# Optimization experiments

Measured on AMD Instinct MI355X. Metric: run time of the kernel, lower is better.

## Reference

```python
import jax, jax.numpy as jnp
import numpy as np

ALPHA = 0.2      # LeakyReLU negative slope for GAT attention
EPS = 1e-6       # LayerNorm eps (custom LayerNorm: (x-mean)/(std+eps)*g+b, unbiased std)
B, L, E, H, D = 16, 1024, 128, 4, 128
N = L + 1        # nodes = codes + appended target node


def leaky(x):
    return jnp.where(x >= 0, x, ALPHA * x)


def layer_norm(x, g, b):
    mu = jnp.mean(x, axis=-1, keepdims=True)
    sd = jnp.std(x, axis=-1, ddof=1, keepdims=True)
    return g * (x - mu) / (sd + EPS) + b


def masked_softmax(logits, mask):
    # logits broadcastable to mask shape [..., N, N]; mask in {0,1}
    l = jnp.where(mask > 0, logits, jnp.asarray(-1e9, logits.dtype))
    a = jax.nn.softmax(l, axis=-1)
    # nodes with no incoming edges aggregate nothing (sparse-GAT semantics)
    has_edge = (jnp.sum(mask, axis=-1, keepdims=True) > 0).astype(a.dtype)
    return a * has_edge


def setup_inputs() -> dict:
    key = jax.random.key(0)
    ks = jax.random.split(key, 20)
    s = 0.1
    HE = H * E
    inp = {}
    inp['data'] = jax.random.randint(ks[0], (B, L), 0, 2).astype(jnp.int32)
    inp['embed'] = jax.random.normal(ks[1], (N, E), jnp.float32) * s
    inp['W_enc'] = jax.random.normal(ks[2], (H, E, E), jnp.float32) * s
    inp['a_enc_src'] = jax.random.normal(ks[3], (H, E), jnp.float32) * s
    inp['a_enc_dst'] = jax.random.normal(ks[4], (H, E), jnp.float32) * s
    inp['g_enc'] = jnp.ones((HE,), jnp.float32)
    inp['b_enc'] = jnp.zeros((HE,), jnp.float32)
    inp['W_dec'] = jax.random.normal(ks[5], (H, HE, D), jnp.float32) * s
    inp['a_dec_src'] = jax.random.normal(ks[6], (H, D), jnp.float32) * s
    inp['a_dec_dst'] = jax.random.normal(ks[7], (H, D), jnp.float32) * s
    inp['g_dec'] = jnp.ones((D,), jnp.float32)
    inp['b_dec'] = jnp.zeros((D,), jnp.float32)
    inp['V_w'] = jax.random.normal(ks[8], (D, D), jnp.float32) * s
    inp['V_b'] = jnp.zeros((D,), jnp.float32)
    inp['o1_w'] = jax.random.normal(ks[9], (D, D), jnp.float32) * s
    inp['o1_b'] = jnp.zeros((D,), jnp.float32)
    inp['o2_w'] = jax.random.normal(ks[10], (D, 1), jnp.float32) * s
    inp['o2_b'] = jnp.zeros((1,), jnp.float32)
    return inp


def reference(data, embed, W_enc, a_enc_src, a_enc_dst, g_enc, b_enc,
              W_dec, a_dec_src, a_dec_dst, g_dec, b_dec,
              V_w, V_b, o1_w, o1_b, o2_w, o2_b):
    emb = embed.at[0].set(0.0)                       # padding_idx=0
    z = (data != 0).astype(emb.dtype)                # [B,L] nonzero indicator
    z_in = jnp.pad(z, ((0, 0), (0, 1)))              # target node absent from input graph
    z_out = jnp.pad(z, ((0, 0), (0, 1)), constant_values=1.0)  # target node added
    mask_in = z_in[:, :, None] * z_in[:, None, :]    # [B,N,N] complete graph over nonzero set
    mask_out = z_out[:, :, None] * z_out[:, None, :]

    # ---- encoder GAT heads (node features shared across batch) ----
    Wh = jnp.einsum('ne,hef->hnf', emb, W_enc)       # [H,N,E]
    f1 = jnp.einsum('hnf,hf->hn', Wh, a_enc_src)
    f2 = jnp.einsum('hnf,hf->hn', Wh, a_enc_dst)
    logits = leaky(f1[:, :, None] + f2[:, None, :])  # [H,N,N], batch-independent
    att = masked_softmax(logits[None], mask_in[:, None])   # [B,H,N,N]
    enc = jax.nn.elu(jnp.einsum('bhij,hjf->bhif', att, Wh))  # concat=True -> ELU
    enc = enc.transpose(0, 2, 1, 3).reshape(data.shape[0], N, -1)  # [B,N,H*E]
    enc = jax.nn.elu(layer_norm(enc, g_enc, b_enc))

    # ---- decoder GAT heads (concat=False -> mean over heads, no ELU) ----
    Wh2 = jnp.einsum('bne,hef->bhnf', enc, W_dec)    # [B,H,N,D]
    g1 = jnp.einsum('bhnf,hf->bhn', Wh2, a_dec_src)
    g2 = jnp.einsum('bhnf,hf->bhn', Wh2, a_dec_dst)
    logits2 = leaky(g1[..., :, None] + g2[..., None, :])   # [B,H,N,N]
    att2 = masked_softmax(logits2, mask_out[:, None])
    dec = jnp.einsum('bhij,bhjf->bhif', att2, Wh2).mean(axis=1)  # [B,N,D]

    dec = jax.nn.relu(layer_norm(dec, g_dec, b_dec)) @ V_w + V_b
    x = dec[:, -1, :]                                # target node per sample
    h = jax.nn.relu(x @ o1_w + o1_b)
    pred = h @ o2_w + o2_b                           # [B,1]
    return pred
```

## Files before the change

kernel.cpp:

```cpp
#include <hip/hip_runtime.h>
#include <hip/hip_bf16.h>

#define BB 16
#define LL 1024
#define EE 128
#define HH 4
#define DD 128
#define NN 1025
#define HE 512
#define AL 0.2f
#define EPSV 1e-6f
#define SS 8
#define CC 128
#define C1 129

#define O_WH   0
#define O_F1   524800
#define O_F2   528900
#define O_ELO  537096
#define O_EHI  541192
#define O_EF1H 545288
#define O_EF1L 549384
#define O_W2   553480
#define O_SLO  555528
#define O_SHI  1612296
#define O_SLOS 2669064
#define O_SHIS 2677320
#define O_WR   2685576
#define O_UP   2751112
#define O_JS   3799688
#define O_PS   3803784
#define O_E4   3807880
#define O_TLO  3807880
#define O_THI  4864648
#define O_TLOS 5921416
#define O_THIS 5929672
#define O_U    4856456
#define O_ZA   4889224
#define O_DP   4889352

__global__ void VGNN_27049704030896_kernel(const float* __restrict__ embed,
                                           const float* __restrict__ W_enc,
                                           const float* __restrict__ a_src,
                                           const float* __restrict__ a_dst,
                                           float* __restrict__ Wh,
                                           float* __restrict__ f1,
                                           float* __restrict__ f2,
                                           float* __restrict__ ef1hi,
                                           float* __restrict__ ef1lo) {
  __shared__ float red[8][EE];
  int n0 = blockIdx.x * 4;
  int h = blockIdx.y;
  int f = threadIdx.x;
  const float* ep0 = embed + (long)((n0 + 0 < NN) ? n0 + 0 : NN - 1) * EE;
  const float* ep1 = embed + (long)((n0 + 1 < NN) ? n0 + 1 : NN - 1) * EE;
  const float* ep2 = embed + (long)((n0 + 2 < NN) ? n0 + 2 : NN - 1) * EE;
  const float* ep3 = embed + (long)((n0 + 3 < NN) ? n0 + 3 : NN - 1) * EE;
  float m0 = (n0 + 0 > 0 && n0 + 0 < NN) ? 1.0f : 0.0f;
  float m1 = (n0 + 1 > 0 && n0 + 1 < NN) ? 1.0f : 0.0f;
  float m2 = (n0 + 2 > 0 && n0 + 2 < NN) ? 1.0f : 0.0f;
  float m3 = (n0 + 3 > 0 && n0 + 3 < NN) ? 1.0f : 0.0f;
  float a0 = 0.0f, a1 = 0.0f, a2 = 0.0f, a3 = 0.0f;
  for (int e = 0; e < EE; e++) {
    float wv = W_enc[((long)(h * EE + e)) * EE + f];
    a0 += ep0[e] * wv; a1 += ep1[e] * wv;
    a2 += ep2[e] * wv; a3 += ep3[e] * wv;
  }
  a0 *= m0; a1 *= m1; a2 *= m2; a3 *= m3;
  if (n0 + 0 < NN) Wh[((long)(h * NN + n0 + 0)) * EE + f] = a0;
  if (n0 + 1 < NN) Wh[((long)(h * NN + n0 + 1)) * EE + f] = a1;
  if (n0 + 2 < NN) Wh[((long)(h * NN + n0 + 2)) * EE + f] = a2;
  if (n0 + 3 < NN) Wh[((long)(h * NN + n0 + 3)) * EE + f] = a3;
  float asv = a_src[h * EE + f];
  float adv = a_dst[h * EE + f];
  red[0][f] = a0 * asv; red[1][f] = a0 * adv;
  red[2][f] = a1 * asv; red[3][f] = a1 * adv;
  red[4][f] = a2 * asv; red[5][f] = a2 * adv;
  red[6][f] = a3 * asv; red[7][f] = a3 * adv;
  __syncthreads();
  for (int s = 64; s > 0; s >>= 1) {
    if (f < s) {
#pragma unroll
      for (int k = 0; k < 8; k++) red[k][f] += red[k][f + s];
    }
    __syncthreads();
  }
  if (f < 4) {
    int n = n0 + f;
    if (n < NN) {
      float v1 = red[2 * f][0];
      float v2 = red[2 * f + 1][0];
      f1[h * NN + n] = v1;
      f2[h * NN + n] = v2;
      if (n < LL) {
        ef1hi[h * LL + n] = expf(v1);
        ef1lo[h * LL + n] = expf(AL * v1);
      }
    }
  }
}

__global__ void k_rank(const float* __restrict__ f2, const float* __restrict__ f1,
                       int* __restrict__ jsort, float* __restrict__ elo,
                       float* __restrict__ ehi, int* __restrict__ pstar) {
  __shared__ float key[LL];
  int h = blockIdx.x;
  int blk = blockIdx.y;
  int t = threadIdx.x;
  for (int q = t; q < LL; q += 128) key[q] = f2[h * NN + q];
  __syncthreads();
  int j0 = blk * 128 + t;
  float kv = key[j0];
  float tg = -f1[h * NN + j0];
  int rank = 0, cnt = 0;
  for (int q = 0; q < LL; q += 4) {
    float4 k4 = *(const float4*)&key[q];
    rank += ((k4.x < kv) || (k4.x == kv && (q + 0) < j0)) ? 1 : 0;
    rank += ((k4.y < kv) || (k4.y == kv && (q + 1) < j0)) ? 1 : 0;
    rank += ((k4.z < kv) || (k4.z == kv && (q + 2) < j0)) ? 1 : 0;
    rank += ((k4.w < kv) || (k4.w == kv && (q + 3) < j0)) ? 1 : 0;
    cnt += (k4.x < tg) ? 1 : 0;
    cnt += (k4.y < tg) ? 1 : 0;
    cnt += (k4.z < tg) ? 1 : 0;
    cnt += (k4.w < tg) ? 1 : 0;
  }
  jsort[h * LL + rank] = j0;
  elo[h * LL + rank] = expf(AL * kv);
  ehi[h * LL + rank] = expf(kv);
  pstar[h * LL + j0] = cnt;
}

__global__ void k_scanA(const int* __restrict__ data, const int* __restrict__ jsort,
                        const float* __restrict__ elo, const float* __restrict__ ehi,
                        const float* __restrict__ Wh,
                        float* __restrict__ TotLo, float* __restrict__ TotHi,
                        float* __restrict__ TotLoS, float* __restrict__ TotHiS) {
  int c = blockIdx.x;
  int h = blockIdx.y;
  int b = blockIdx.z;
  int t = threadIdx.x;
  int bh = b * HH + h;
  float al0 = 0.0f, al1 = 0.0f, ah0 = 0.0f, ah1 = 0.0f, sl = 0.0f, sh = 0.0f;
  for (int r = 0; r < SS; r++) {
    int p = c * SS + r;
    int j = jsort[h * LL + p];
    if (data[b * LL + j] != 0) {
      float wl = elo[h * LL + p];
      float wh = ehi[h * LL + p];
      float2 v = *(const float2*)&Wh[((long)(h * NN + j)) * EE + 2 * t];
      al0 += wl * v.x; al1 += wl * v.y;
      ah0 += wh * v.x; ah1 += wh * v.y;
      sl += wl; sh += wh;
    }
  }
  long o = (long)(bh * C1 + c);
  float2 s;
  s.x = al0; s.y = al1; *(float2*)&TotLo[o * EE + 2 * t] = s;
  s.x = ah0; s.y = ah1; *(float2*)&TotHi[o * EE + 2 * t] = s;
  if (t == 0) { TotLoS[o] = sl; TotHiS[o] = sh; }
}

__global__ void k_scanB(const float* __restrict__ TotLo, const float* __restrict__ TotHi,
                        const float* __restrict__ TotLoS, const float* __restrict__ TotHiS,
                        float* __restrict__ SnapLo, float* __restrict__ SnapHi,
                        float* __restrict__ SnapLoS, float* __restrict__ SnapHiS) {
  int bh = blockIdx.x;
  int f = threadIdx.x & 127;
  int a = threadIdx.x >> 7;
  const float* __restrict__ T  = a ? TotHi  : TotLo;
  const float* __restrict__ Ts = a ? TotHiS : TotLoS;
  float* __restrict__ S  = a ? SnapHi  : SnapLo;
  float* __restrict__ Ss = a ? SnapHiS : SnapLoS;
  float r = 0.0f, rs = 0.0f;
#pragma unroll 8
  for (int c = 0; c < CC; c++) {
    long o = (long)(bh * C1 + c);
    float tv = T[o * EE + f];
    float ts = Ts[o];
    S[o * EE + f] = r;
    if (f == 0) Ss[o] = rs;
    r += tv; rs += ts;
  }
  long o = (long)(bh * C1 + CC);
  S[o * EE + f] = r;
  if (f == 0) Ss[o] = rs;
}

__global__ void k_w2(const float* __restrict__ W_dec, const float* __restrict__ a_vec,
                     float* __restrict__ w2) {
  int k = blockIdx.x * 128 + threadIdx.x;
  int h = blockIdx.y;
  const float4* wp = (const float4*)&W_dec[(long)(h * HE + k) * DD];
  const float4* ap = (const float4*)&a_vec[h * DD];
  float s = 0.0f;
  for (int d = 0; d < DD / 4; d++) {
    float4 wv = wp[d];
    float4 av = ap[d];
    s += wv.x * av.x + wv.y * av.y + wv.z * av.z + wv.w * av.w;
  }
  w2[h * HE + k] = s;
}

__global__ void k_row(const int* __restrict__ data, const float* __restrict__ Wh,
                      const int* __restrict__ pstar, const int* __restrict__ jsort,
                      const float* __restrict__ elo, const float* __restrict__ ehi,
                      const float* __restrict__ ef1hi, const float* __restrict__ ef1lo,
                      const float* __restrict__ SnapLo, const float* __restrict__ SnapHi,
                      const float* __restrict__ SnapLoS, const float* __restrict__ SnapHiS,
                      const float* __restrict__ g_enc, const float* __restrict__ b_enc,
                      const float* __restrict__ w2,
                      __hip_bfloat16* __restrict__ enc4, float* __restrict__ wrow) {
  int i = blockIdx.x;
  int b = blockIdx.y;
  int t = threadIdx.x;
  if (data[b * LL + i] == 0) {
    if (t < HH) wrow[(b * HH + t) * LL + i] = 0.0f;
    return;
  }
  float x0[HH];
  float x1[HH];
  for (int h = 0; h < HH; h++) {
    int p = pstar[h * LL + i];
    int c = p / SS;
    int bh = b * HH + h;
    long o = (long)(bh * C1 + c);
    float2 rl = *(const float2*)&SnapLo[o * EE + 2 * t];
    float2 rh = *(const float2*)&SnapHi[o * EE + 2 * t];
    float rls = SnapLoS[o];
    float rhs = SnapHiS[o];
    int q0 = c * SS;
    int np = p - q0;
#pragma unroll
    for (int r = 0; r < 7; r++) {
      if (r < np) {
        int j = jsort[h * LL + q0 + r];
        if (data[b * LL + j] != 0) {
          float wl = elo[h * LL + q0 + r];
          float wh2 = ehi[h * LL + q0 + r];
          float2 v = *(const float2*)&Wh[((long)(h * NN + j)) * EE + 2 * t];
          rl.x += wl * v.x; rl.y += wl * v.y;
          rh.x += wh2 * v.x; rh.y += wh2 * v.y;
          rls += wl; rhs += wh2;
        }
      }
    }
    long ot = (long)(bh * C1 + CC);
    float2 Th = *(const float2*)&SnapHi[ot * EE + 2 * t];
    float Ths = SnapHiS[ot];
    float eh = ef1hi[h * LL + i];
    float el = ef1lo[h * LL + i];
    float den = 1.0f / (eh * (Ths - rhs) + el * rls);
    float v0 = (eh * (Th.x - rh.x) + el * rl.x) * den;
    float v1 = (eh * (Th.y - rh.y) + el * rl.y) * den;
    x0[h] = (v0 > 0.0f) ? v0 : (expf(v0) - 1.0f);
    x1[h] = (v1 > 0.0f) ? v1 : (expf(v1) - 1.0f);
  }
  float loc = 0.0f;
  for (int h = 0; h < HH; h++) loc += x0[h] + x1[h];
#pragma unroll
  for (int s = 1; s < 64; s <<= 1) loc += __shfl_xor(loc, s, 64);
  float mu = loc * (1.0f / 512.0f);
  float q2 = 0.0f;
  for (int h = 0; h < HH; h++) {
    float d0 = x0[h] - mu;
    float d1 = x1[h] - mu;
    q2 += d0 * d0 + d1 * d1;
  }
#pragma unroll
  for (int s = 1; s < 64; s <<= 1) q2 += __shfl_xor(q2, s, 64);
  float inv = 1.0f / (sqrtf(q2 * (1.0f / 511.0f)) + EPSV);
  float e40[HH];
  float e41[HH];
  long rowo = ((long)(b * LL + i)) * HE;
  for (int h = 0; h < HH; h++) {
    float2 g = *(const float2*)&g_enc[h * EE + 2 * t];
    float2 bb = *(const float2*)&b_enc[h * EE + 2 * t];
    float v0 = g.x * (x0[h] - mu) * inv + bb.x;
    float v1 = g.y * (x1[h] - mu) * inv + bb.y;
    e40[h] = (v0 > 0.0f) ? v0 : (expf(v0) - 1.0f);
    e41[h] = (v1 > 0.0f) ? v1 : (expf(v1) - 1.0f);
    __hip_bfloat162 pk;
    pk.x = __float2bfloat16(e40[h]);
    pk.y = __float2bfloat16(e41[h]);
    *(__hip_bfloat162*)&enc4[rowo + h * EE + 2 * t] = pk;
  }
  float p0 = 0.0f, p1 = 0.0f, p2 = 0.0f, p3 = 0.0f;
  for (int h = 0; h < HH; h++) {
    float2 wA = *(const float2*)&w2[0 * HE + h * EE + 2 * t];
    float2 wB = *(const float2*)&w2[1 * HE + h * EE + 2 * t];
    float2 wC = *(const float2*)&w2[2 * HE + h * EE + 2 * t];
    float2 wD = *(const float2*)&w2[3 * HE + h * EE + 2 * t];
    p0 += e40[h] * wA.x + e41[h] * wA.y;
    p1 += e40[h] * wB.x + e41[h] * wB.y;
    p2 += e40[h] * wC.x + e41[h] * wC.y;
    p3 += e40[h] * wD.x + e41[h] * wD.y;
  }
#pragma unroll
  for (int s = 1; s < 64; s <<= 1) {
    p0 += __shfl_xor(p0, s, 64);
    p1 += __shfl_xor(p1, s, 64);
    p2 += __shfl_xor(p2, s, 64);
    p3 += __shfl_xor(p3, s, 64);
  }
  if (t < HH) {
    float g = (t == 0) ? p0 : (t == 1) ? p1 : (t == 2) ? p2 : p3;
    if (g < 0.0f) g *= AL;
    wrow[(b * HH + t) * LL + i] = expf(g);
  }
}

__global__ void k_acc(const int* __restrict__ data, const __hip_bfloat16* __restrict__ enc4,
                      const float* __restrict__ wrow, float* __restrict__ Upart) {
  int c = blockIdx.x;
  int b = blockIdx.y;
  int t = threadIdx.x;
  float a00 = 0.0f, a01 = 0.0f, a10 = 0.0f, a11 = 0.0f;
  float a20 = 0.0f, a21 = 0.0f, a30 = 0.0f, a31 = 0.0f;
  for (int r = 0; r < 64; r++) {
    int i = c * 64 + r;
    if (data[b * LL + i] == 0) continue;
    float w0 = wrow[(b * HH + 0) * LL + i];
    float w1 = wrow[(b * HH + 1) * LL + i];
    float w2v = wrow[(b * HH + 2) * LL + i];
    float w3 = wrow[(b * HH + 3) * LL + i];
    __hip_bfloat162 pk = *(const __hip_bfloat162*)&enc4[((long)(b * LL + i)) * HE + 2 * t];
    float e0 = __bfloat162float(pk.x);
    float e1 = __bfloat162float(pk.y);
    a00 += w0 * e0; a01 += w0 * e1;
    a10 += w1 * e0; a11 += w1 * e1;
    a20 += w2v * e0; a21 += w2v * e1;
    a30 += w3 * e0; a31 += w3 * e1;
  }
  long base = (long)(b * 16 + c) * (HH * HE);
  float2 s;
  s.x = a00; s.y = a01; *(float2*)&Upart[base + 0 * HE + 2 * t] = s;
  s.x = a10; s.y = a11; *(float2*)&Upart[base + 1 * HE + 2 * t] = s;
  s.x = a20; s.y = a21; *(float2*)&Upart[base + 2 * HE + 2 * t] = s;
  s.x = a30; s.y = a31; *(float2*)&Upart[base + 3 * HE + 2 * t] = s;
}

__global__ void k_usum(const float* __restrict__ Upart, const float* __restrict__ wrow,
                       float* __restrict__ U, float* __restrict__ zacc) {
  __shared__ float red[256];
  int b = blockIdx.x;
  int t = threadIdx.x;
  for (int k = t; k < HH * HE; k += 256) {
    float s = 0.0f;
    for (int c = 0; c < 16; c++) {
      s += Upart[(long)(b * 16 + c) * (HH * HE) + k];
    }
    U[b * (HH * HE) + k] = s;
  }
  for (int hp = 0; hp < HH; hp++) {
    float p = 0.0f;
    for (int q = t; q < LL; q += 256) p += wrow[(b * HH + hp) * LL + q];
    red[t] = p;
    __syncthreads();
    for (int s = 128; s > 0; s >>= 1) {
      if (t < s) red[t] += red[t + s];
      __syncthreads();
    }
    if (t == 0) zacc[b * HH + hp] = red[0];
    __syncthreads();
  }
}

__global__ void k_dmv(const float* __restrict__ U, const float* __restrict__ zacc,
                      const float* __restrict__ W_dec, float* __restrict__ decPart) {
  __shared__ float Uc[128];
  int cK = blockIdx.x;
  int b = blockIdx.y;
  int f = threadIdx.x;
  int k0 = cK * 128;
  int h = cK / 4;
  Uc[f] = U[b * (HH * HE) + k0 + f];
  __syncthreads();
  float zinv = 1.0f / (1.0f + zacc[b * HH + h]);
  float s = 0.0f;
  for (int kk = 0; kk < 128; kk++) {
    s += Uc[kk] * W_dec[(long)(k0 + kk) * DD + f];
  }
  decPart[(long)(b * 16 + cK) * DD + f] = 0.25f * s * zinv;
}

__global__ void k_finB(const float* __restrict__ decPart,
                       const float* __restrict__ g_dec, const float* __restrict__ b_dec,
                       const float* __restrict__ V_w, const float* __restrict__ V_b,
                       const float* __restrict__ o1_w, const float* __restrict__ o1_b,
                       const float* __restrict__ o2_w, const float* __restrict__ o2_b,
                       float* __restrict__ out) {
  __shared__ float red[DD];
  __shared__ float xs[DD];
  int b = blockIdx.x;
  int f = threadIdx.x;
  float dec = 0.0f;
  for (int cK = 0; cK < 16; cK++) {
    dec += decPart[(long)(b * 16 + cK) * DD + f];
  }
  red[f] = dec;
  __syncthreads();
  for (int s = 64; s > 0; s >>= 1) {
    if (f < s) red[f] += red[f + s];
    __syncthreads();
  }
  float mu = red[0] / 128.0f;
  __syncthreads();
  float dd = dec - mu;
  red[f] = dd * dd;
  __syncthreads();
  for (int s = 64; s > 0; s >>= 1) {
    if (f < s) red[f] += red[f + s];
    __syncthreads();
  }
  float sd = sqrtf(red[0] / 127.0f);
  float t = g_dec[f] * dd / (sd + EPSV) + b_dec[f];
  if (t < 0.0f) t = 0.0f;
  __syncthreads();
  xs[f] = t;
  __syncthreads();
  float xv = 0.0f;
  for (int k = 0; k < DD; k++) xv += xs[k] * V_w[k * DD + f];
  xv += V_b[f];
  __syncthreads();
  xs[f] = xv;
  __syncthreads();
  float hv = 0.0f;
  for (int k = 0; k < DD; k++) hv += xs[k] * o1_w[k * DD + f];
  hv += o1_b[f];
  if (hv < 0.0f) hv = 0.0f;
  red[f] = hv * o2_w[f];
  __syncthreads();
  for (int s = 64; s > 0; s >>= 1) {
    if (f < s) red[f] += red[f + s];
    __syncthreads();
  }
  if (f == 0) out[b] = red[0] + o2_b[0];
}

extern "C" void kernel_launch(void* const* d_in, const int* in_sizes, int n_in,
                              void* d_out, int out_size, void* d_ws, size_t ws_size,
                              hipStream_t stream) {
  const int* data    = (const int*)d_in[0];
  const float* embed  = (const float*)d_in[1];
  const float* W_enc  = (const float*)d_in[2];
  const float* a_esrc = (const float*)d_in[3];
  const float* a_edst = (const float*)d_in[4];
  const float* g_enc  = (const float*)d_in[5];
  const float* b_enc  = (const float*)d_in[6];
  const float* W_dec  = (const float*)d_in[7];
  const float* a_ddst = (const float*)d_in[9];
  const float* g_dec  = (const float*)d_in[10];
  const float* b_dec  = (const float*)d_in[11];
  const float* V_w    = (const float*)d_in[12];
  const float* V_b    = (const float*)d_in[13];
  const float* o1_w   = (const float*)d_in[14];
  const float* o1_b   = (const float*)d_in[15];
  const float* o2_w   = (const float*)d_in[16];
  const float* o2_b   = (const float*)d_in[17];
  float* out = (float*)d_out;

  float* w = (float*)d_ws;
  float* Wh    = w + O_WH;
  float* f1    = w + O_F1;
  float* f2    = w + O_F2;
  float* elo   = w + O_ELO;
  float* ehi   = w + O_EHI;
  float* ef1hi = w + O_EF1H;
  float* ef1lo = w + O_EF1L;
  float* w2    = w + O_W2;
  float* SnapLo  = w + O_SLO;
  float* SnapHi  = w + O_SHI;
  float* SnapLoS = w + O_SLOS;
  float* SnapHiS = w + O_SHIS;
  float* TotLo   = w + O_TLO;
  float* TotHi   = w + O_THI;
  float* TotLoS  = w + O_TLOS;
  float* TotHiS  = w + O_THIS;
  float* wrow  = w + O_WR;
  float* Upart = w + O_UP;
  int* jsort   = (int*)(w + O_JS);
  int* pstar   = (int*)(w + O_PS);
  __hip_bfloat16* enc4 = (__hip_bfloat16*)(w + O_E4);
  float* U     = w + O_U;
  float* zacc  = w + O_ZA;
  float* decPart = w + O_DP;

  VGNN_27049704030896_kernel<<<dim3((NN + 3) / 4, HH), 128, 0, stream>>>(
      embed, W_enc, a_esrc, a_edst, Wh, f1, f2, ef1hi, ef1lo);
  k_rank<<<dim3(HH, LL / 128), 128, 0, stream>>>(f2, f1, jsort, elo, ehi, pstar);
  k_scanA<<<dim3(CC, HH, BB), 64, 0, stream>>>(data, jsort, elo, ehi, Wh,
                                               TotLo, TotHi, TotLoS, TotHiS);
  k_scanB<<<BB * HH, 256, 0, stream>>>(TotLo, TotHi, TotLoS, TotHiS,
                                       SnapLo, SnapHi, SnapLoS, SnapHiS);
  k_w2  <<<dim3(HE / 128, HH), 128, 0, stream>>>(W_dec, a_ddst, w2);
  k_row <<<dim3(LL, BB), 64, 0, stream>>>(data, Wh, pstar, jsort, elo, ehi,
                                          ef1hi, ef1lo, SnapLo, SnapHi,
                                          SnapLoS, SnapHiS, g_enc, b_enc, w2,
                                          enc4, wrow);
  k_acc <<<dim3(16, BB), 256, 0, stream>>>(data, enc4, wrow, Upart);
  k_usum<<<BB, 256, 0, stream>>>(Upart, wrow, U, zacc);
  k_dmv <<<dim3(16, BB), 128, 0, stream>>>(U, zacc, W_dec, decPart);
  k_finB<<<BB, 128, 0, stream>>>(decPart, g_dec, b_dec, V_w, V_b,
                                 o1_w, o1_b, o2_w, o2_b, out);
}
```

Measured before the change: 237.6 us.

## Fuse decoder tail kernels into one per-batch block and merge w2 into rank

Merges the k_w2 projection into the rank kernel as extra blocks. Replaces four tail kernels (accumulate, partial sum, decoder matvec, final MLP) with a single 1024-thread block per batch that reduces in shared memory. This removes several launches and global round-trips for partial buffers. In exchange, the enc4 accumulation now runs on only 16 blocks instead of 256, which reduces parallelism over a large memory read.

```diff
diff --git a/kernel.cpp b/kernel.cpp
--- a/kernel.cpp
+++ b/kernel.cpp
@@ -27,7 +27,6 @@
 #define O_SLOS 2669064
 #define O_SHIS 2677320
 #define O_WR   2685576
-#define O_UP   2751112
 #define O_JS   3799688
 #define O_PS   3803784
 #define O_E4   3807880
@@ -35,9 +34,6 @@
 #define O_THI  4864648
 #define O_TLOS 5921416
 #define O_THIS 5929672
-#define O_U    4856456
-#define O_ZA   4889224
-#define O_DP   4889352
 
 __global__ void VGNN_27049704030896_kernel(const float* __restrict__ embed,
                                            const float* __restrict__ W_enc,
@@ -100,13 +96,31 @@
   }
 }
 
-__global__ void k_rank(const float* __restrict__ f2, const float* __restrict__ f1,
-                       int* __restrict__ jsort, float* __restrict__ elo,
-                       float* __restrict__ ehi, int* __restrict__ pstar) {
+__global__ void k_rankw2(const float* __restrict__ f2, const float* __restrict__ f1,
+                         const float* __restrict__ W_dec, const float* __restrict__ a_vec,
+                         int* __restrict__ jsort, float* __restrict__ elo,
+                         float* __restrict__ ehi, int* __restrict__ pstar,
+                         float* __restrict__ w2) {
+  int gx = blockIdx.x;
+  int t = threadIdx.x;
+  if (gx >= 32) {
+    int idx = gx - 32;
+    int h = idx >> 2;
+    int k = (idx & 3) * 128 + t;
+    const float4* wp = (const float4*)&W_dec[(long)(h * HE + k) * DD];
+    const float4* ap = (const float4*)&a_vec[h * DD];
+    float s = 0.0f;
+    for (int d = 0; d < DD / 4; d++) {
+      float4 wv = wp[d];
+      float4 av = ap[d];
+      s += wv.x * av.x + wv.y * av.y + wv.z * av.z + wv.w * av.w;
+    }
+    w2[h * HE + k] = s;
+    return;
+  }
   __shared__ float key[LL];
-  int h = blockIdx.x;
-  int blk = blockIdx.y;
-  int t = threadIdx.x;
+  int h = gx & 3;
+  int blk = gx >> 2;
   for (int q = t; q < LL; q += 128) key[q] = f2[h * NN + q];
   __syncthreads();
   int j0 = blk * 128 + t;
@@ -184,21 +198,6 @@
   long o = (long)(bh * C1 + CC);
   S[o * EE + f] = r;
   if (f == 0) Ss[o] = rs;
-}
-
-__global__ void k_w2(const float* __restrict__ W_dec, const float* __restrict__ a_vec,
-                     float* __restrict__ w2) {
-  int k = blockIdx.x * 128 + threadIdx.x;
-  int h = blockIdx.y;
-  const float4* wp = (const float4*)&W_dec[(long)(h * HE + k) * DD];
-  const float4* ap = (const float4*)&a_vec[h * DD];
-  float s = 0.0f;
-  for (int d = 0; d < DD / 4; d++) {
-    float4 wv = wp[d];
-    float4 av = ap[d];
-    s += wv.x * av.x + wv.y * av.y + wv.z * av.z + wv.w * av.w;
-  }
-  w2[h * HE + k] = s;
 }
 
 __global__ void k_row(const int* __restrict__ data, const float* __restrict__ Wh,
@@ -309,21 +308,35 @@
   }
 }
 
-__global__ void k_acc(const int* __restrict__ data, const __hip_bfloat16* __restrict__ enc4,
-                      const float* __restrict__ wrow, float* __restrict__ Upart) {
-  int c = blockIdx.x;
-  int b = blockIdx.y;
+__global__ __launch_bounds__(1024) void k_tail(
+    const int* __restrict__ data, const __hip_bfloat16* __restrict__ enc4,
+    const float* __restrict__ wrow, const float* __restrict__ W_dec,
+    const float* __restrict__ g_dec, const float* __restrict__ b_dec,
+    const float* __restrict__ V_w, const float* __restrict__ V_b,
+    const float* __restrict__ o1_w, const float* __restrict__ o1_b,
+    const float* __restrict__ o2_w, const float* __restrict__ o2_b,
+    float* __restrict__ out) {
+  __shared__ float P[4][HH * HE];
+  __shared__ float Ut[HH * HE];
+  __shared__ float zr[4][256];
+  __shared__ float zs[4];
+  __shared__ float red8[8][DD];
+  __shared__ float red[DD];
+  __shared__ float xs[DD];
+  int b = blockIdx.x;
   int t = threadIdx.x;
+  int rg = t >> 8;
+  int tt = t & 255;
   float a00 = 0.0f, a01 = 0.0f, a10 = 0.0f, a11 = 0.0f;
   float a20 = 0.0f, a21 = 0.0f, a30 = 0.0f, a31 = 0.0f;
-  for (int r = 0; r < 64; r++) {
-    int i = c * 64 + r;
+  for (int r = 0; r < 256; r++) {
+    int i = r * 4 + rg;
     if (data[b * LL + i] == 0) continue;
     float w0 = wrow[(b * HH + 0) * LL + i];
     float w1 = wrow[(b * HH + 1) * LL + i];
     float w2v = wrow[(b * HH + 2) * LL + i];
     float w3 = wrow[(b * HH + 3) * LL + i];
-    __hip_bfloat162 pk = *(const __hip_bfloat162*)&enc4[((long)(b * LL + i)) * HE + 2 * t];
+    __hip_bfloat162 pk = *(const __hip_bfloat162*)&enc4[((long)(b * LL + i)) * HE + 2 * tt];
     float e0 = __bfloat162float(pk.x);
     float e1 = __bfloat162float(pk.y);
     a00 += w0 * e0; a01 += w0 * e1;
@@ -331,110 +344,109 @@
     a20 += w2v * e0; a21 += w2v * e1;
     a30 += w3 * e0; a31 += w3 * e1;
   }
-  long base = (long)(b * 16 + c) * (HH * HE);
-  float2 s;
-  s.x = a00; s.y = a01; *(float2*)&Upart[base + 0 * HE + 2 * t] = s;
-  s.x = a10; s.y = a11; *(float2*)&Upart[base + 1 * HE + 2 * t] = s;
-  s.x = a20; s.y = a21; *(float2*)&Upart[base + 2 * HE + 2 * t] = s;
-  s.x = a30; s.y = a31; *(float2*)&Upart[base + 3 * HE + 2 * t] = s;
-}
-
-__global__ void k_usum(const float* __restrict__ Upart, const float* __restrict__ wrow,
-                       float* __restrict__ U, float* __restrict__ zacc) {
-  __shared__ float red[256];
-  int b = blockIdx.x;
-  int t = threadIdx.x;
-  for (int k = t; k < HH * HE; k += 256) {
+  P[rg][0 * HE + 2 * tt] = a00; P[rg][0 * HE + 2 * tt + 1] = a01;
+  P[rg][1 * HE + 2 * tt] = a10; P[rg][1 * HE + 2 * tt + 1] = a11;
+  P[rg][2 * HE + 2 * tt] = a20; P[rg][2 * HE + 2 * tt + 1] = a21;
+  P[rg][3 * HE + 2 * tt] = a30; P[rg][3 * HE + 2 * tt + 1] = a31;
+  float zp = wrow[(b * HH + rg) * LL + tt]
+           + wrow[(b * HH + rg) * LL + tt + 256]
+           + wrow[(b * HH + rg) * LL + tt + 512]
+           + wrow[(b * HH + rg) * LL + tt + 768];
+  zr[rg][tt] = zp;
+  __syncthreads();
+  int wid = t >> 6;
+  int lane = t & 63;
+  if (wid < 4) {
+    float s = zr[wid][lane] + zr[wid][lane + 64] + zr[wid][lane + 128] + zr[wid][lane + 192];
+#pragma unroll
+    for (int d = 1; d < 64; d <<= 1) s += __shfl_xor(s, d, 64);
+    if (lane == 0) zs[wid] = 0.25f / (1.0f + s);
+  }
+  __syncthreads();
+  for (int k2 = t; k2 < HH * HE; k2 += 1024) {
+    int h2 = k2 >> 9;
+    Ut[k2] = (P[0][k2] + P[1][k2] + P[2][k2] + P[3][k2]) * zs[h2];
+  }
+  __syncthreads();
+  int f = t & 127;
+  int kg = t >> 7;
+  {
     float s = 0.0f;
-    for (int c = 0; c < 16; c++) {
-      s += Upart[(long)(b * 16 + c) * (HH * HE) + k];
+    int k0 = kg * 256;
+#pragma unroll 8
+    for (int kk = k0; kk < k0 + 256; kk++) {
+      s += Ut[kk] * W_dec[(long)kk * DD + f];
     }
-    U[b * (HH * HE) + k] = s;
-  }
-  for (int hp = 0; hp < HH; hp++) {
-    float p = 0.0f;
-    for (int q = t; q < LL; q += 256) p += wrow[(b * HH + hp) * LL + q];
-    red[t] = p;
+    red8[kg][f] = s;
+  }
+  __syncthreads();
+  float dec = 0.0f;
+  if (t < DD) {
+#pragma unroll
+    for (int g = 0; g < 8; g++) dec += red8[g][t];
+    red[t] = dec;
+  }
+  __syncthreads();
+  for (int s = 64; s > 0; s >>= 1) {
+    if (t < s) red[t] += red[t + s];
     __syncthreads();
-    for (int s = 128; s > 0; s >>= 1) {
-      if (t < s) red[t] += red[t + s];
-      __syncthreads();
-    }
-    if (t == 0) zacc[b * HH + hp] = red[0];
+  }
+  float mu = red[0] / 128.0f;
+  __syncthreads();
+  float dd = 0.0f;
+  if (t < DD) { dd = dec - mu; red[t] = dd * dd; }
+  __syncthreads();
+  for (int s = 64; s > 0; s >>= 1) {
+    if (t < s) red[t] += red[t + s];
     __syncthreads();
   }
-}
-
-__global__ void k_dmv(const float* __restrict__ U, const float* __restrict__ zacc,
-                      const float* __restrict__ W_dec, float* __restrict__ decPart) {
-  __shared__ float Uc[128];
-  int cK = blockIdx.x;
-  int b = blockIdx.y;
-  int f = threadIdx.x;
-  int k0 = cK * 128;
-  int h = cK / 4;
-  Uc[f] = U[b * (HH * HE) + k0 + f];
-  __syncthreads();
-  float zinv = 1.0f / (1.0f + zacc[b * HH + h]);
-  float s = 0.0f;
-  for (int kk = 0; kk < 128; kk++) {
-    s += Uc[kk] * W_dec[(long)(k0 + kk) * DD + f];
-  }
-  decPart[(long)(b * 16 + cK) * DD + f] = 0.25f * s * zinv;
-}
-
-__global__ void k_finB(const float* __restrict__ decPart,
-                       const float* __restrict__ g_dec, const float* __restrict__ b_dec,
-                       const float* __restrict__ V_w, const float* __restrict__ V_b,
-                       const float* __restrict__ o1_w, const float* __restrict__ o1_b,
-                       const float* __restrict__ o2_w, const float* __restrict__ o2_b,
-                       float* __restrict__ out) {
-  __shared__ float red[DD];
-  __shared__ float xs[DD];
-  int b = blockIdx.x;
-  int f = threadIdx.x;
-  float dec = 0.0f;
-  for (int cK = 0; cK < 16; cK++) {
-    dec += decPart[(long)(b * 16 + cK) * DD + f];
-  }
-  red[f] = dec;
+  float sd = sqrtf(red[0] / 127.0f);
+  __syncthreads();
+  if (t < DD) {
+    float v = g_dec[t] * dd / (sd + EPSV) + b_dec[t];
+    if (v < 0.0f) v = 0.0f;
+    xs[t] = v;
+  }
+  __syncthreads();
+  {
+    float s = 0.0f;
+    int k0 = kg * 16;
+#pragma unroll
+    for (int k = k0; k < k0 + 16; k++) s += xs[k] * V_w[k * DD + f];
+    red8[kg][f] = s;
+  }
+  __syncthreads();
+  float xv = 0.0f;
+  if (t < DD) {
+#pragma unroll
+    for (int g = 0; g < 8; g++) xv += red8[g][t];
+    xv += V_b[t];
+  }
+  __syncthreads();
+  if (t < DD) xs[t] = xv;
+  __syncthreads();
+  {
+    float s = 0.0f;
+    int k0 = kg * 16;
+#pragma unroll
+    for (int k = k0; k < k0 + 16; k++) s += xs[k] * o1_w[k * DD + f];
+    red8[kg][f] = s;
+  }
+  __syncthreads();
+  if (t < DD) {
+    float hv = 0.0f;
+#pragma unroll
+    for (int g = 0; g < 8; g++) hv += red8[g][t];
+    hv += o1_b[t];
+    if (hv < 0.0f) hv = 0.0f;
+    red[t] = hv * o2_w[t];
+  }
   __syncthreads();
   for (int s = 64; s > 0; s >>= 1) {
-    if (f < s) red[f] += red[f + s];
+    if (t < s) red[t] += red[t + s];
     __syncthreads();
   }
-  float mu = red[0] / 128.0f;
-  __syncthreads();
-  float dd = dec - mu;
-  red[f] = dd * dd;
-  __syncthreads();
-  for (int s = 64; s > 0; s >>= 1) {
-    if (f < s) red[f] += red[f + s];
-    __syncthreads();
-  }
-  float sd = sqrtf(red[0] / 127.0f);
-  float t = g_dec[f] * dd / (sd + EPSV) + b_dec[f];
-  if (t < 0.0f) t = 0.0f;
-  __syncthreads();
-  xs[f] = t;
-  __syncthreads();
-  float xv = 0.0f;
-  for (int k = 0; k < DD; k++) xv += xs[k] * V_w[k * DD + f];
-  xv += V_b[f];
-  __syncthreads();
-  xs[f] = xv;
-  __syncthreads();
-  float hv = 0.0f;
-  for (int k = 0; k < DD; k++) hv += xs[k] * o1_w[k * DD + f];
-  hv += o1_b[f];
-  if (hv < 0.0f) hv = 0.0f;
-  red[f] = hv * o2_w[f];
-  __syncthreads();
-  for (int s = 64; s > 0; s >>= 1) {
-    if (f < s) red[f] += red[f + s];
-    __syncthreads();
-  }
-  if (f == 0) out[b] = red[0] + o2_b[0];
+  if (t == 0) out[b] = red[0] + o2_b[0];
 }
 
 extern "C" void kernel_launch(void* const* d_in, const int* in_sizes, int n_in,
@@ -477,29 +489,23 @@
   float* TotLoS  = w + O_TLOS;
   float* TotHiS  = w + O_THIS;
   float* wrow  = w + O_WR;
-  float* Upart = w + O_UP;
   int* jsort   = (int*)(w + O_JS);
   int* pstar   = (int*)(w + O_PS);
   __hip_bfloat16* enc4 = (__hip_bfloat16*)(w + O_E4);
-  float* U     = w + O_U;
-  float* zacc  = w + O_ZA;
-  float* decPart = w + O_DP;
 
   VGNN_27049704030896_kernel<<<dim3((NN + 3) / 4, HH), 128, 0, stream>>>(
       embed, W_enc, a_esrc, a_edst, Wh, f1, f2, ef1hi, ef1lo);
-  k_rank<<<dim3(HH, LL / 128), 128, 0, stream>>>(f2, f1, jsort, elo, ehi, pstar);
+  k_rankw2<<<48, 128, 0, stream>>>(f2, f1, W_dec, a_ddst,
+                                   jsort, elo, ehi, pstar, w2);
   k_scanA<<<dim3(CC, HH, BB), 64, 0, stream>>>(data, jsort, elo, ehi, Wh,
                                                TotLo, TotHi, TotLoS, TotHiS);
   k_scanB<<<BB * HH, 256, 0, stream>>>(TotLo, TotHi, TotLoS, TotHiS,
                                        SnapLo, SnapHi, SnapLoS, SnapHiS);
-  k_w2  <<<dim3(HE / 128, HH), 128, 0, stream>>>(W_dec, a_ddst, w2);
   k_row <<<dim3(LL, BB), 64, 0, stream>>>(data, Wh, pstar, jsort, elo, ehi,
                                           ef1hi, ef1lo, SnapLo, SnapHi,
                                           SnapLoS, SnapHiS, g_enc, b_enc, w2,
                                           enc4, wrow);
-  k_acc <<<dim3(16, BB), 256, 0, stream>>>(data, enc4, wrow, Upart);
-  k_usum<<<BB, 256, 0, stream>>>(Upart, wrow, U, zacc);
-  k_dmv <<<dim3(16, BB), 128, 0, stream>>>(U, zacc, W_dec, decPart);
-  k_finB<<<BB, 128, 0, stream>>>(decPart, g_dec, b_dec, V_w, V_b,
-                                 o1_w, o1_b, o2_w, o2_b, out);
-}
+  k_tail<<<BB, 1024, 0, stream>>>(data, enc4, wrow, W_dec,
+                                  g_dec, b_dec, V_w, V_b,
+                                  o1_w, o1_b, o2_w, o2_b, out);
+}
```

After: 308.5 us. 1.3x slower.
